# Performance work log

Measured on AMD Instinct MI355X. Metric: run time of the kernel, lower is better.

Reference implementation:

```python
import jax, jax.numpy as jnp
import numpy as np

N_BOTTLENECK = 256  # must be a power of two for the butterfly network


def butterfly_ortho(x, theta, first_output_entry_positive=False):
    """FFT-like butterfly of Givens rotations over the last dim (size n, power of 2).
    Stage s pairs indices (i, i + 2^s); each pair gets one rotation angle.
    theta has (n/2)*log2(n) entries, consumed stage by stage.
    """
    n = x.shape[-1]
    stages = int(np.log2(n))
    idx = 0
    for s in range(stages):
        stride = 1 << s
        nb = n // (2 * stride)
        th = theta[idx: idx + n // 2].reshape(nb, stride)
        idx += n // 2
        xr = x.reshape(-1, nb, 2, stride)  # [B, blocks, half, offset]
        a, b = xr[:, :, 0, :], xr[:, :, 1, :]
        c, sn = jnp.cos(th), jnp.sin(th)
        a2 = c * a - sn * b
        b2 = sn * a + c * b
        x = jnp.stack([a2, b2], axis=2).reshape(-1, n)
    if first_output_entry_positive:
        # convention flag: force sign of first output entry non-negative
        x = x.at[:, 0].set(jnp.abs(x[:, 0]))
    return x


def setup_inputs() -> dict:
    key = jax.random.key(0)
    ks = jax.random.split(key, 12)
    dims = [4096, 1024, 256, 1024, 4096]
    B = 16384

    def w(k, i, o):
        return (jax.random.normal(k, (i, o), dtype=jnp.float32) * (1.0 / np.sqrt(i)))

    inp = {
        "x": jax.random.normal(ks[0], (B, dims[0]), dtype=jnp.float32),
        "enc_w0": w(ks[1], dims[0], dims[1]),
        "enc_b0": jnp.zeros((dims[1],), jnp.float32),
        "enc_w1": w(ks[2], dims[1], dims[2]),
        "enc_b1": jnp.zeros((dims[2],), jnp.float32),
        "theta": jax.random.normal(ks[3], ((dims[2] // 2) * int(np.log2(dims[2])),), dtype=jnp.float32),
        "dec_w0": w(ks[4], dims[2], dims[3]),
        "dec_b0": jnp.zeros((dims[3],), jnp.float32),
        "out_w": w(ks[5], dims[3], dims[4]),
        "out_b": jnp.zeros((dims[4],), jnp.float32),
    }
    return inp


def reference(x, enc_w0, enc_b0, enc_w1, enc_b1, theta, dec_w0, dec_b0, out_w, out_b):
    # encoder: Linear + ReLU stack
    h = jax.nn.relu(x @ enc_w0 + enc_b0)
    h = jax.nn.relu(h @ enc_w1 + enc_b1)
    # orthogonal butterfly network at the bottleneck
    h = butterfly_ortho(h, theta, first_output_entry_positive=False)
    # decoder: Linear + ReLU stack, then plain Linear output layer
    h = jax.nn.relu(h @ dec_w0 + dec_b0)
    out = h @ out_w + out_b
    return out
```

## Files before the change

kernel.cpp:

```cpp
#include <hip/hip_runtime.h>

typedef __attribute__((ext_vector_type(8))) short short8v;
typedef __attribute__((ext_vector_type(4))) float f32x4;
typedef __attribute__((ext_vector_type(4))) unsigned int uint4v;
typedef __attribute__((ext_vector_type(4))) float float4v;

__device__ __forceinline__ unsigned short f2bf(float f) {
  union { float f; unsigned u; } v; v.f = f;
  unsigned r = v.u + 0x7fffu + ((v.u >> 16) & 1u);
  return (unsigned short)(r >> 16);
}
__device__ __forceinline__ float bf2f(unsigned short h) {
  union { unsigned u; float f; } v; v.u = ((unsigned)h) << 16;
  return v.f;
}
__device__ __forceinline__ unsigned pack2(float a, float b) {
  return (unsigned)f2bf(a) | ((unsigned)f2bf(b) << 16);
}

__device__ __forceinline__ void gload_lds16(const void* g, void* l) {
  __builtin_amdgcn_global_load_lds(
      (const __attribute__((address_space(1))) void*)g,
      (__attribute__((address_space(3))) void*)l, 16, 0, 0);
}

#define SBAR() __builtin_amdgcn_s_barrier()
#define SCHED0() __builtin_amdgcn_sched_barrier(0)
#define LGKM(n) do { asm volatile("s_waitcnt lgkmcnt(" #n ")" ::: "memory"); \
                     __builtin_amdgcn_sched_barrier(0); } while (0)
#define VMW(n) asm volatile("s_waitcnt vmcnt(" #n ")" ::: "memory")

__global__ void f32_to_bf16(const float* __restrict__ in, unsigned short* __restrict__ out,
                            size_t n8) {
  size_t i = (size_t)blockIdx.x * blockDim.x + threadIdx.x;
  const size_t stride = (size_t)gridDim.x * blockDim.x;
  for (; i < n8; i += stride) {
    const float4v* p = (const float4v*)(in + i * 8);
    float4v a = __builtin_nontemporal_load(p);
    float4v b = __builtin_nontemporal_load(p + 1);
    uint4v r;
    r.x = pack2(a.x, a.y); r.y = pack2(a.z, a.w);
    r.z = pack2(b.x, b.y); r.w = pack2(b.z, b.w);
    *(uint4v*)(out + i * 8) = r;
  }
}

__global__ void transpose_bf16(const float* __restrict__ W, unsigned short* __restrict__ WT,
                               int K, int N) {
  __shared__ float t[32][33];
  const int kb = blockIdx.x * 32, nb = blockIdx.y * 32;
  const int tx = threadIdx.x, ty = threadIdx.y;
  #pragma unroll
  for (int y = 0; y < 4; ++y)
    t[ty + y*8][tx] = W[(size_t)(kb + ty + y*8) * N + nb + tx];
  __syncthreads();
  #pragma unroll
  for (int y = 0; y < 4; ++y) {
    const int n = nb + ty + y*8;
    WT[(size_t)n * K + kb + tx] = f2bf(t[tx][ty + y*8]);
  }
}

__global__ void trig_kernel(const float* __restrict__ theta, float* __restrict__ ct,
                            float* __restrict__ st, int n) {
  const int i = blockIdx.x * 256 + threadIdx.x;
  if (i < n) {
    float s, c;
    sincosf(theta[i], &s, &c);
    ct[i] = c; st[i] = s;
  }
}

__global__ void butterfly_kernel(const unsigned short* __restrict__ X,
                                 unsigned short* __restrict__ Y,
                                 const float* __restrict__ ct, const float* __restrict__ st) {
  __shared__ float L[2][256];
  const int tid = threadIdx.x;
  const size_t base = (size_t)blockIdx.x * 512;
  const unsigned v = *(const unsigned*)(X + base + tid * 2);
  const int r = tid >> 7;
  const int col = (tid * 2) & 255;
  L[r][col]     = bf2f((unsigned short)(v & 0xffffu));
  L[r][col + 1] = bf2f((unsigned short)(v >> 16));
  __syncthreads();
  const int p = tid & 127;
  #pragma unroll
  for (int s = 0; s < 8; ++s) {
    const int stride = 1 << s;
    const int t = p & (stride - 1);
    const int i = ((p >> s) << (s + 1)) + t;
    const int j = i + stride;
    const float c  = ct[s * 128 + p];
    const float sn = st[s * 128 + p];
    const float a = L[r][i], b = L[r][j];
    L[r][i] = c * a - sn * b;
    L[r][j] = sn * a + c * b;
    __syncthreads();
  }
  const unsigned lo = f2bf(L[r][col]);
  const unsigned hi = f2bf(L[r][col + 1]);
  *(unsigned*)(Y + base + tid * 2) = lo | (hi << 16);
}

template<bool RELU, bool OUT_F32>
__global__ __launch_bounds__(256) void gemm_kernel(
    const unsigned short* __restrict__ A, const unsigned short* __restrict__ BT,
    const float* __restrict__ bias, void* __restrict__ Cp,
    int M, int N, int K)
{
  __shared__ __align__(16) unsigned short As[128 * 32];
  __shared__ __align__(16) unsigned short Bs[128 * 32];
  const int tid = threadIdx.x;
  const int lane = tid & 63;
  const int w = tid >> 6;
  const int wm = w >> 1, wn = w & 1;
  const int n0 = blockIdx.x * 128;
  const int m0 = blockIdx.y * 128;
  const int g4 = lane >> 4;
  const int ml = lane & 15;

  f32x4 acc[4][4];
  #pragma unroll
  for (int i = 0; i < 4; ++i)
    #pragma unroll
    for (int n = 0; n < 4; ++n)
      #pragma unroll
      for (int e = 0; e < 4; ++e)
        acc[i][n][e] = 0.0f;

  const int nkt = K >> 5;
  const int srow = w * 32 + (lane >> 2);
  const int scol = (lane & 3) * 8;

  for (int kt = 0; kt < nkt; ++kt) {
    const int k0 = kt << 5;
    #pragma unroll
    for (int q = 0; q < 2; ++q) {
      const unsigned short* gb = BT + (size_t)(n0 + srow + q * 16) * K + k0 + scol;
      gload_lds16(gb, Bs + w * 1024 + q * 512);
      const unsigned short* ga = A + (size_t)(m0 + srow + q * 16) * K + k0 + scol;
      gload_lds16(ga, As + w * 1024 + q * 512);
    }
    __syncthreads();
    short8v af[4], bf[4];
    #pragma unroll
    for (int i = 0; i < 4; ++i)
      af[i] = *(const short8v*)(As + (wm * 64 + i * 16 + ml) * 32 + g4 * 8);
    #pragma unroll
    for (int n = 0; n < 4; ++n)
      bf[n] = *(const short8v*)(Bs + (wn * 64 + n * 16 + ml) * 32 + g4 * 8);
    #pragma unroll
    for (int i = 0; i < 4; ++i)
      #pragma unroll
      for (int n = 0; n < 4; ++n)
        acc[i][n] = __builtin_amdgcn_mfma_f32_16x16x32_bf16(af[i], bf[n], acc[i][n], 0, 0, 0);
    __syncthreads();
  }
  #pragma unroll
  for (int n = 0; n < 4; ++n) {
    const int col = n0 + wn * 64 + n * 16 + ml;
    const float bv = bias[col];
    #pragma unroll
    for (int i = 0; i < 4; ++i) {
      const int rowb = m0 + wm * 64 + i * 16 + g4 * 4;
      #pragma unroll
      for (int r = 0; r < 4; ++r) {
        float v = acc[i][n][r] + bv;
        if constexpr (RELU) v = fmaxf(v, 0.0f);
        if constexpr (OUT_F32)
          __builtin_nontemporal_store(v, &((float*)Cp)[(size_t)(rowb + r) * N + col]);
        else
          ((unsigned short*)Cp)[(size_t)(rowb + r) * N + col] = f2bf(v);
      }
    }
  }
}

template<int MI0, int NI0>
__device__ __forceinline__ void mfma8(f32x4 (&acc)[8][4], const short8v (&a)[4],
                                      const short8v (&b)[2]) {
  __builtin_amdgcn_s_setprio(1);
  #pragma unroll
  for (int mi = 0; mi < 4; ++mi)
    #pragma unroll
    for (int ni = 0; ni < 2; ++ni)
      acc[MI0+mi][NI0+ni] = __builtin_amdgcn_mfma_f32_16x16x32_bf16(
          a[mi], b[ni], acc[MI0+mi][NI0+ni], 0, 0, 0);
  __builtin_amdgcn_s_setprio(0);
}

template<bool RELU, bool OUT_F32>
__global__ __launch_bounds__(512, 2) void gemm256(
    const unsigned short* __restrict__ A, const unsigned short* __restrict__ BT,
    const float* __restrict__ bias, void* __restrict__ Cp,
    int M, int N, int K)
{
  __shared__ __align__(16) unsigned char lds[131072];
  const int tid = threadIdx.x;
  const int lane = tid & 63, w = tid >> 6;
  const int wm = w >> 2, wn = w & 3;
  const int ml = lane & 15, g4 = lane >> 4;

  const int nx = gridDim.x;
  const int nwg = nx * (int)gridDim.y;
  const int bid = blockIdx.y * nx + blockIdx.x;
  const int cpx = nwg >> 3;
  const int swz = (bid & 7) * cpx + (bid >> 3);
  const int n0 = (swz % nx) * 256;
  const int m0 = (swz / nx) * 256;

  const int rloc = w * 8 + (lane >> 3);
  const int scol = ((lane & 7) ^ (lane >> 3)) * 8;
  const int ldst = w * 1024;

  const int off0 = (g4 * 16) ^ ((ml & 7) << 4);
  const int aoff = (wm * 128 + ml) * 128 + off0;
  const int boff = (wn * 64 + ml) * 128 + off0;

  const int NT = K >> 6;
  const int NJ = NT >> 1;

  f32x4 acc[8][4];
  #pragma unroll
  for (int mi = 0; mi < 8; ++mi)
    #pragma unroll
    for (int ni = 0; ni < 4; ++ni)
      #pragma unroll
      for (int e = 0; e < 4; ++e)
        acc[mi][ni][e] = 0.0f;

  auto stA = [&](int d, int h, int t) {
    const unsigned short* g0 = A + (size_t)(m0 + h * 128 + rloc) * K + t * 64 + scol;
    unsigned char* l0 = lds + d * 65536 + h * 16384 + ldst;
    gload_lds16(g0, l0);
    gload_lds16(g0 + (size_t)64 * K, l0 + 8192);
  };
  auto stB = [&](int d, int h, int t) {
    const unsigned short* g0 = BT + (size_t)(n0 + h * 128 + rloc) * K + t * 64 + scol;
    unsigned char* l0 = lds + d * 65536 + 32768 + h * 16384 + ldst;
    gload_lds16(g0, l0);
    gload_lds16(g0 + (size_t)64 * K, l0 + 8192);
  };
  auto rdA0 = [&](short8v (&dst)[4], int d, int mh) {
    #pragma unroll
    for (int mi = 0; mi < 4; ++mi)
      dst[mi] = *(const short8v*)(lds + d * 65536 + aoff + (mh * 4 + mi) * 2048);
  };
  auto rdA1 = [&](short8v (&dst)[4], int d, int mh) {
    #pragma unroll
    for (int mi = 0; mi < 4; ++mi)
      dst[mi] = *(const short8v*)(lds + ((d * 65536 + aoff + (mh * 4 + mi) * 2048) ^ 64));
  };
  auto rdB0 = [&](short8v (&dst)[2], int d, int nh) {
    #pragma unroll
    for (int ni = 0; ni < 2; ++ni)
      dst[ni] = *(const short8v*)(lds + d * 65536 + 32768 + boff + (nh * 2 + ni) * 2048);
  };
  auto rdB1 = [&](short8v (&dst)[2], int d, int nh) {
    #pragma unroll
    for (int ni = 0; ni < 2; ++ni)
      dst[ni] = *(const short8v*)(lds + ((d * 65536 + 32768 + boff + (nh * 2 + ni) * 2048) ^ 64));
  };

  short8v aR_0[4], aR_1[4], aS_0[4], aS_1[4];
  short8v bR0_0[2], bR0_1[2], bR1_0[2], bR1_1[2];

  stB(0, 0, 0); stB(0, 1, 0); stA(0, 0, 0); stA(0, 1, 0);
  stB(1, 0, 1); stB(1, 1, 1);
  VMW(4);
  SBAR();

  for (int j = 0; j < NJ; ++j) {
    const int t1 = 2 * j + 1;
    const int t2 = (2 * j + 2 < NT) ? 2 * j + 2 : NT - 1;
    const int t3 = (2 * j + 3 < NT) ? 2 * j + 3 : NT - 1;

    rdB0(bR0_0, 0, 0); rdA0(aR_0, 0, 0);
    SCHED0();
    rdB1(bR0_1, 0, 0); rdA1(aR_1, 0, 0);
    stA(1, 0, t1);
    SBAR(); LGKM(6);
    mfma8<0, 0>(acc, aR_0, bR0_0);
    LGKM(0);
    mfma8<0, 0>(acc, aR_1, bR0_1);
    SBAR();
    rdB0(bR1_0, 0, 1);
    SCHED0();
    rdB1(bR1_1, 0, 1);
    stA(1, 1, t1);
    SBAR(); LGKM(2);
    mfma8<0, 2>(acc, aR_0, bR1_0);
    LGKM(0);
    mfma8<0, 2>(acc, aR_1, bR1_1);
    SBAR();
    rdA0(aS_0, 0, 1);
    SCHED0();
    rdA1(aS_1, 0, 1);
    stB(0, 0, t2);
    SBAR(); LGKM(4);
    mfma8<4, 0>(acc, aS_0, bR0_0);
    LGKM(0);
    mfma8<4, 0>(acc, aS_1, bR0_1);
    SBAR();
    stB(0, 1, t2);
    SBAR();
    mfma8<4, 2>(acc, aS_0, bR1_0);
    mfma8<4, 2>(acc, aS_1, bR1_1);
    VMW(4);
    SBAR();

    rdB0(bR0_0, 1, 0); rdA0(aR_0, 1, 0);
    SCHED0();
    rdB1(bR0_1, 1, 0); rdA1(aR_1, 1, 0);
    stA(0, 0, t2);
    SBAR(); LGKM(6);
    mfma8<0, 0>(acc, aR_0, bR0_0);
    LGKM(0);
    mfma8<0, 0>(acc, aR_1, bR0_1);
    SBAR();
    rdB0(bR1_0, 1, 1);
    SCHED0();
    rdB1(bR1_1, 1, 1);
    stA(0, 1, t2);
    SBAR(); LGKM(2);
    mfma8<0, 2>(acc, aR_0, bR1_0);
    LGKM(0);
    mfma8<0, 2>(acc, aR_1, bR1_1);
    SBAR();
    rdA0(aS_0, 1, 1);
    SCHED0();
    rdA1(aS_1, 1, 1);
    stB(1, 0, t3);
    SBAR(); LGKM(4);
    mfma8<4, 0>(acc, aS_0, bR0_0);
    LGKM(0);
    mfma8<4, 0>(acc, aS_1, bR0_1);
    SBAR();
    stB(1, 1, t3);
    SBAR();
    mfma8<4, 2>(acc, aS_0, bR1_0);
    mfma8<4, 2>(acc, aS_1, bR1_1);
    VMW(4);
    SBAR();
  }

  #pragma unroll
  for (int ni = 0; ni < 4; ++ni) {
    const int col = n0 + wn * 64 + ni * 16 + ml;
    const float bv = bias[col];
    #pragma unroll
    for (int mi = 0; mi < 8; ++mi) {
      const int rowb = m0 + wm * 128 + mi * 16 + g4 * 4;
      #pragma unroll
      for (int r = 0; r < 4; ++r) {
        float v = acc[mi][ni][r] + bv;
        if constexpr (RELU) v = fmaxf(v, 0.0f);
        if constexpr (OUT_F32)
          __builtin_nontemporal_store(v, &((float*)Cp)[(size_t)(rowb + r) * N + col]);
        else
          ((unsigned short*)Cp)[(size_t)(rowb + r) * N + col] = f2bf(v);
      }
    }
  }
}

extern "C" void kernel_launch(void* const* d_in, const int* in_sizes, int n_in,
                              void* d_out, int out_size, void* d_ws, size_t ws_size,
                              hipStream_t stream) {
  const float* x      = (const float*)d_in[0];
  const float* enc_w0 = (const float*)d_in[1];
  const float* enc_b0 = (const float*)d_in[2];
  const float* enc_w1 = (const float*)d_in[3];
  const float* enc_b1 = (const float*)d_in[4];
  const float* theta  = (const float*)d_in[5];
  const float* dec_w0 = (const float*)d_in[6];
  const float* dec_b0 = (const float*)d_in[7];
  const float* out_w  = (const float*)d_in[8];
  const float* out_b  = (const float*)d_in[9];
  float* out = (float*)d_out;

  char* ws = (char*)d_ws;
  unsigned short* xb  = (unsigned short*)(ws);
  unsigned short* wt0 = (unsigned short*)(ws + 134217728);
  unsigned short* wt1 = (unsigned short*)(ws + 142606336);
  unsigned short* wt2 = (unsigned short*)(ws + 143130624);
  unsigned short* wt3 = (unsigned short*)(ws + 143654912);
  unsigned short* h1  = (unsigned short*)(ws + 152043520);
  unsigned short* h2  = (unsigned short*)(ws + 185597952);
  unsigned short* h2b = (unsigned short*)(ws + 193986560);
  unsigned short* h3  = h1;
  float* ct = (float*)(ws + 202375168);
  float* st = ct + 1024;

  const int B = 16384;

  f32_to_bf16<<<2048, 256, 0, stream>>>(x, xb, (size_t)B * 4096 / 8);
  transpose_bf16<<<dim3(4096/32, 1024/32), dim3(32, 8), 0, stream>>>(enc_w0, wt0, 4096, 1024);
  transpose_bf16<<<dim3(1024/32,  256/32), dim3(32, 8), 0, stream>>>(enc_w1, wt1, 1024, 256);
  transpose_bf16<<<dim3( 256/32, 1024/32), dim3(32, 8), 0, stream>>>(dec_w0, wt2, 256, 1024);
  transpose_bf16<<<dim3(1024/32, 4096/32), dim3(32, 8), 0, stream>>>(out_w,  wt3, 1024, 4096);
  trig_kernel<<<4, 256, 0, stream>>>(theta, ct, st, 1024);

  gemm256<true,  false><<<dim3(1024/256, B/256), 512, 0, stream>>>(xb, wt0, enc_b0, h1, B, 1024, 4096);
  gemm_kernel<true,  false><<<dim3( 256/128, B/128), 256, 0, stream>>>(h1, wt1, enc_b1, h2, B, 256, 1024);
  butterfly_kernel<<<B/2, 256, 0, stream>>>(h2, h2b, ct, st);
  gemm_kernel<true,  false><<<dim3(1024/128, B/128), 256, 0, stream>>>(h2b, wt2, dec_b0, h3, B, 1024, 256);
  gemm256<false, true ><<<dim3(4096/256, B/256), 512, 0, stream>>>(h3, wt3, out_b, out, B, 4096, 1024);
}
```

Baseline: 394.0 us.

## Fuse bottleneck GEMM, butterfly, and decoder GEMM into one kernel

Replaces the second encoder GEMM, the butterfly kernel and the first decoder GEMM with a single kernel. Each block takes 64 rows, computes the 256-wide bottleneck in fp32 inside a swizzled 64KB LDS tile, applies all 8 butterfly stages in LDS, then streams dec_w0 in 128-column chunks to produce h3. This removes the global round trips for h2/h2b and two kernel launches. In exchange it uses 128KB of LDS per block, which limits occupancy to one block per CU, has no load/compute overlap, and runs a serial butterfly loop per thread with per-stage barriers. It also keeps the bottleneck in fp32 rather than rounding it to bf16 before the butterfly.

```diff
diff --git a/kernel.cpp b/kernel.cpp
--- a/kernel.cpp
+++ b/kernel.cpp
@@ -71,106 +71,156 @@
   }
 }
 
-__global__ void butterfly_kernel(const unsigned short* __restrict__ X,
-                                 unsigned short* __restrict__ Y,
-                                 const float* __restrict__ ct, const float* __restrict__ st) {
-  __shared__ float L[2][256];
+__global__ __launch_bounds__(256) void midfused(
+    const unsigned short* __restrict__ h1, const unsigned short* __restrict__ wt1,
+    const float* __restrict__ b1, const unsigned short* __restrict__ wt2,
+    const float* __restrict__ b2, const float* __restrict__ ct,
+    const float* __restrict__ st, unsigned short* __restrict__ h3)
+{
+  __shared__ __align__(16) unsigned char lds[131072];
+  unsigned short* As = (unsigned short*)(lds + 65536);
+  unsigned short* Bs = (unsigned short*)(lds + 65536 + 4096);
+
   const int tid = threadIdx.x;
-  const size_t base = (size_t)blockIdx.x * 512;
-  const unsigned v = *(const unsigned*)(X + base + tid * 2);
-  const int r = tid >> 7;
-  const int col = (tid * 2) & 255;
-  L[r][col]     = bf2f((unsigned short)(v & 0xffffu));
-  L[r][col + 1] = bf2f((unsigned short)(v >> 16));
+  const int lane = tid & 63, w = tid >> 6;
+  const int wm = w >> 1, wn = w & 1;
+  const int ml = lane & 15, g4 = lane >> 4;
+  const int r0 = blockIdx.x * 64;
+
+  f32x4 acc[2][8];
+  #pragma unroll
+  for (int mi = 0; mi < 2; ++mi)
+    #pragma unroll
+    for (int ni = 0; ni < 8; ++ni)
+      #pragma unroll
+      for (int e = 0; e < 4; ++e)
+        acc[mi][ni][e] = 0.0f;
+
+  const int srl = lane >> 2;
+  const int scol = (lane & 3) * 8;
+
+  for (int kt = 0; kt < 32; ++kt) {
+    const int k0 = kt * 32;
+    gload_lds16(h1 + (size_t)(r0 + w * 16 + srl) * 1024 + k0 + scol, As + w * 512);
+    #pragma unroll
+    for (int q = 0; q < 4; ++q)
+      gload_lds16(wt1 + (size_t)(w * 64 + q * 16 + srl) * 1024 + k0 + scol,
+                  Bs + w * 2048 + q * 512);
+    VMW(0);
+    __syncthreads();
+    short8v af[2], bf[8];
+    #pragma unroll
+    for (int mi = 0; mi < 2; ++mi)
+      af[mi] = *(const short8v*)(As + (wm * 32 + mi * 16 + ml) * 32 + g4 * 8);
+    #pragma unroll
+    for (int ni = 0; ni < 8; ++ni)
+      bf[ni] = *(const short8v*)(Bs + (wn * 128 + ni * 16 + ml) * 32 + g4 * 8);
+    #pragma unroll
+    for (int mi = 0; mi < 2; ++mi)
+      #pragma unroll
+      for (int ni = 0; ni < 8; ++ni)
+        acc[mi][ni] = __builtin_amdgcn_mfma_f32_16x16x32_bf16(af[mi], bf[ni], acc[mi][ni], 0, 0, 0);
+    __syncthreads();
+  }
+  #pragma unroll
+  for (int ni = 0; ni < 8; ++ni) {
+    const int col = wn * 128 + ni * 16 + ml;
+    const float bv = b1[col];
+    #pragma unroll
+    for (int mi = 0; mi < 2; ++mi) {
+      #pragma unroll
+      for (int r = 0; r < 4; ++r) {
+        const int row = wm * 32 + mi * 16 + g4 * 4 + r;
+        const float v = fmaxf(acc[mi][ni][r] + bv, 0.0f);
+        *(float*)(lds + row * 1024 + ((col * 4) ^ ((row & 7) << 5))) = v;
+      }
+    }
+  }
   __syncthreads();
-  const int p = tid & 127;
-  #pragma unroll
-  for (int s = 0; s < 8; ++s) {
-    const int stride = 1 << s;
-    const int t = p & (stride - 1);
-    const int i = ((p >> s) << (s + 1)) + t;
-    const int j = i + stride;
-    const float c  = ct[s * 128 + p];
-    const float sn = st[s * 128 + p];
-    const float a = L[r][i], b = L[r][j];
-    L[r][i] = c * a - sn * b;
-    L[r][j] = sn * a + c * b;
+
+  {
+    const int rr = tid >> 2;
+    const int qq = tid & 3;
+    const int xr = (rr & 7) << 5;
+    #pragma unroll
+    for (int s = 0; s < 8; ++s) {
+      const int stride = 1 << s;
+      for (int k = 0; k < 32; ++k) {
+        const int p = qq * 32 + k;
+        const int i = ((p >> s) << (s + 1)) + (p & (stride - 1));
+        const int j = i + stride;
+        float* pa = (float*)(lds + rr * 1024 + ((i * 4) ^ xr));
+        float* pb = (float*)(lds + rr * 1024 + ((j * 4) ^ xr));
+        const float a = *pa, bb = *pb;
+        const float c = ct[s * 128 + p], sn = st[s * 128 + p];
+        *pa = c * a - sn * bb;
+        *pb = sn * a + c * bb;
+      }
+      __syncthreads();
+    }
+  }
+
+  unsigned char* B2 = lds + 65536;
+  for (int nb = 0; nb < 8; ++nb) {
     __syncthreads();
-  }
-  const unsigned lo = f2bf(L[r][col]);
-  const unsigned hi = f2bf(L[r][col + 1]);
-  *(unsigned*)(Y + base + tid * 2) = lo | (hi << 16);
-}
-
-template<bool RELU, bool OUT_F32>
-__global__ __launch_bounds__(256) void gemm_kernel(
-    const unsigned short* __restrict__ A, const unsigned short* __restrict__ BT,
-    const float* __restrict__ bias, void* __restrict__ Cp,
-    int M, int N, int K)
-{
-  __shared__ __align__(16) unsigned short As[128 * 32];
-  __shared__ __align__(16) unsigned short Bs[128 * 32];
-  const int tid = threadIdx.x;
-  const int lane = tid & 63;
-  const int w = tid >> 6;
-  const int wm = w >> 1, wn = w & 1;
-  const int n0 = blockIdx.x * 128;
-  const int m0 = blockIdx.y * 128;
-  const int g4 = lane >> 4;
-  const int ml = lane & 15;
-
-  f32x4 acc[4][4];
-  #pragma unroll
-  for (int i = 0; i < 4; ++i)
-    #pragma unroll
-    for (int n = 0; n < 4; ++n)
-      #pragma unroll
-      for (int e = 0; e < 4; ++e)
-        acc[i][n][e] = 0.0f;
-
-  const int nkt = K >> 5;
-  const int srow = w * 32 + (lane >> 2);
-  const int scol = (lane & 3) * 8;
-
-  for (int kt = 0; kt < nkt; ++kt) {
-    const int k0 = kt << 5;
-    #pragma unroll
-    for (int q = 0; q < 2; ++q) {
-      const unsigned short* gb = BT + (size_t)(n0 + srow + q * 16) * K + k0 + scol;
-      gload_lds16(gb, Bs + w * 1024 + q * 512);
-      const unsigned short* ga = A + (size_t)(m0 + srow + q * 16) * K + k0 + scol;
-      gload_lds16(ga, As + w * 1024 + q * 512);
-    }
+    #pragma unroll
+    for (int c = 0; c < 16; ++c) {
+      const int k = w * 16 + c;
+      const int rloc = 2 * k + (lane >> 5);
+      const int g = lane & 31;
+      const unsigned short* src = wt2 + (size_t)(nb * 128 + rloc) * 256
+                                      + ((g ^ (rloc & 7)) * 8);
+      gload_lds16(src, B2 + k * 1024);
+    }
+    VMW(0);
     __syncthreads();
-    short8v af[4], bf[4];
-    #pragma unroll
-    for (int i = 0; i < 4; ++i)
-      af[i] = *(const short8v*)(As + (wm * 64 + i * 16 + ml) * 32 + g4 * 8);
-    #pragma unroll
-    for (int n = 0; n < 4; ++n)
-      bf[n] = *(const short8v*)(Bs + (wn * 64 + n * 16 + ml) * 32 + g4 * 8);
-    #pragma unroll
-    for (int i = 0; i < 4; ++i)
-      #pragma unroll
-      for (int n = 0; n < 4; ++n)
-        acc[i][n] = __builtin_amdgcn_mfma_f32_16x16x32_bf16(af[i], bf[n], acc[i][n], 0, 0, 0);
-    __syncthreads();
-  }
-  #pragma unroll
-  for (int n = 0; n < 4; ++n) {
-    const int col = n0 + wn * 64 + n * 16 + ml;
-    const float bv = bias[col];
-    #pragma unroll
-    for (int i = 0; i < 4; ++i) {
-      const int rowb = m0 + wm * 64 + i * 16 + g4 * 4;
-      #pragma unroll
-      for (int r = 0; r < 4; ++r) {
-        float v = acc[i][n][r] + bv;
-        if constexpr (RELU) v = fmaxf(v, 0.0f);
-        if constexpr (OUT_F32)
-          __builtin_nontemporal_store(v, &((float*)Cp)[(size_t)(rowb + r) * N + col]);
-        else
-          ((unsigned short*)Cp)[(size_t)(rowb + r) * N + col] = f2bf(v);
+
+    f32x4 acc2[2][4];
+    #pragma unroll
+    for (int mi = 0; mi < 2; ++mi)
+      #pragma unroll
+      for (int ni = 0; ni < 4; ++ni)
+        #pragma unroll
+        for (int e = 0; e < 4; ++e)
+          acc2[mi][ni][e] = 0.0f;
+
+    #pragma unroll
+    for (int kt = 0; kt < 8; ++kt) {
+      const int c0 = kt * 32 + g4 * 8;
+      short8v af2[2], bf2[4];
+      #pragma unroll
+      for (int mi = 0; mi < 2; ++mi) {
+        const int arow = wm * 32 + mi * 16 + ml;
+        const unsigned char* ap = lds + arow * 1024 + ((c0 * 4) ^ ((arow & 7) << 5));
+        float4v x0 = *(const float4v*)ap;
+        float4v x1 = *(const float4v*)(ap + 16);
+        uint4v u;
+        u.x = pack2(x0.x, x0.y); u.y = pack2(x0.z, x0.w);
+        u.z = pack2(x1.x, x1.y); u.w = pack2(x1.z, x1.w);
+        af2[mi] = *(short8v*)&u;
+      }
+      #pragma unroll
+      for (int ni = 0; ni < 4; ++ni) {
+        const int brow = wn * 64 + ni * 16 + ml;
+        bf2[ni] = *(const short8v*)(B2 + brow * 512 + ((c0 * 2) ^ ((brow & 7) << 4)));
+      }
+      #pragma unroll
+      for (int mi = 0; mi < 2; ++mi)
+        #pragma unroll
+        for (int ni = 0; ni < 4; ++ni)
+          acc2[mi][ni] = __builtin_amdgcn_mfma_f32_16x16x32_bf16(af2[mi], bf2[ni], acc2[mi][ni], 0, 0, 0);
+    }
+    #pragma unroll
+    for (int ni = 0; ni < 4; ++ni) {
+      const int colg = nb * 128 + wn * 64 + ni * 16 + ml;
+      const float bv = b2[colg];
+      #pragma unroll
+      for (int mi = 0; mi < 2; ++mi) {
+        #pragma unroll
+        for (int r = 0; r < 4; ++r) {
+          const int rowg = r0 + wm * 32 + mi * 16 + g4 * 4 + r;
+          h3[(size_t)rowg * 1024 + colg] = f2bf(fmaxf(acc2[mi][ni][r] + bv, 0.0f));
+        }
       }
     }
   }
@@ -386,10 +436,8 @@
   unsigned short* wt2 = (unsigned short*)(ws + 143130624);
   unsigned short* wt3 = (unsigned short*)(ws + 143654912);
   unsigned short* h1  = (unsigned short*)(ws + 152043520);
-  unsigned short* h2  = (unsigned short*)(ws + 185597952);
-  unsigned short* h2b = (unsigned short*)(ws + 193986560);
-  unsigned short* h3  = h1;
-  float* ct = (float*)(ws + 202375168);
+  unsigned short* h3  = (unsigned short*)(ws + 185597952);
+  float* ct = (float*)(ws + 219152384);
   float* st = ct + 1024;
 
   const int B = 16384;
@@ -402,8 +450,6 @@
   trig_kernel<<<4, 256, 0, stream>>>(theta, ct, st, 1024);
 
   gemm256<true,  false><<<dim3(1024/256, B/256), 512, 0, stream>>>(xb, wt0, enc_b0, h1, B, 1024, 4096);
-  gemm_kernel<true,  false><<<dim3( 256/128, B/128), 256, 0, stream>>>(h1, wt1, enc_b1, h2, B, 256, 1024);
-  butterfly_kernel<<<B/2, 256, 0, stream>>>(h2, h2b, ct, st);
-  gemm_kernel<true,  false><<<dim3(1024/128, B/128), 256, 0, stream>>>(h2b, wt2, dec_b0, h3, B, 1024, 256);
+  midfused<<<B/64, 256, 0, stream>>>(h1, wt1, enc_b1, wt2, dec_b0, ct, st, h3);
   gemm256<false, true ><<<dim3(4096/256, B/256), 512, 0, stream>>>(h3, wt3, out_b, out, B, 4096, 1024);
 }
```

Result: slower. 418.9 us (+6.3%).
